# Optimization experiments

Measured on AMD Instinct MI355X. Metric: run time of the kernel, lower is better.

The kernel has to match this reference:

```python
import jax, jax.numpy as jnp
import numpy as np
from jax import lax

DIM = 2048
NUM_HEADS = 16
HEAD_DIM = DIM // NUM_HEADS  # 128
BLOCK = 128
EPS = 1e-6


def setup_inputs() -> dict:
    key = jax.random.key(0)
    kq, kk, kv = jax.random.split(key, 3)
    B, S = 2, 4096
    q = jax.random.normal(kq, (B, S, DIM), dtype=jnp.float32)
    k = jax.random.normal(kk, (B, S, DIM), dtype=jnp.float32)
    v = jax.random.normal(kv, (B, S, DIM), dtype=jnp.float32)
    return {"q": q, "k": k, "v": v}


def _flash_attn(q, k, v):
    # q,k,v: [B, S, DIM] -> [B, H, S, Dh]
    B, S, _ = q.shape
    def split_heads(x):
        return jnp.transpose(x.reshape(B, -1, NUM_HEADS, HEAD_DIM), (0, 2, 1, 3))
    scale = HEAD_DIM ** (-0.5)
    qh = split_heads(q) * scale  # pre-scale, as in original __call__
    kh = split_heads(k)
    vh = split_heads(v)
    Sk = kh.shape[2]
    num_chunks = (Sk + BLOCK - 1) // BLOCK

    o0 = jnp.zeros((B, NUM_HEADS, S, HEAD_DIM), dtype=jnp.float32)
    l0 = jnp.zeros((B, NUM_HEADS, S, 1), dtype=jnp.float32)
    m0 = jnp.full((B, NUM_HEADS, S, 1), -jnp.inf, dtype=jnp.float32)

    def chunk_scanner(carry, chunk_idx):
        o, l, m_run = carry
        start = chunk_idx * BLOCK
        k_c = lax.dynamic_slice(kh, (0, 0, start, 0), (B, NUM_HEADS, BLOCK, HEAD_DIM))
        v_c = lax.dynamic_slice(vh, (0, 0, start, 0), (B, NUM_HEADS, BLOCK, HEAD_DIM))
        # scores: [B, H, Sq, BLOCK]; note second division by sqrt(head_dim) (faithful)
        s = jnp.einsum('bhqd,bhkd->bhqk', qh, k_c,
                       precision=lax.Precision.HIGHEST) / jnp.sqrt(jnp.float32(HEAD_DIM))
        m_chunk = jnp.max(s, axis=-1, keepdims=True)
        m_new = jnp.maximum(m_run, m_chunk)
        exp_scale = jnp.exp(m_run - m_new)
        exp_s = jnp.exp(s - m_chunk)  # faithful: uses m_chunk, not m_new
        l_new = l * exp_scale + jnp.sum(exp_s, axis=-1, keepdims=True)
        o_chunk = jnp.einsum('bhqk,bhkd->bhqd', exp_s, v_c,
                             precision=lax.Precision.HIGHEST)
        o_new = o * exp_scale + o_chunk
        return (o_new, l_new, m_new), None

    (o, l, _), _ = lax.scan(chunk_scanner, (o0, l0, m0), jnp.arange(num_chunks))
    o = o / (l + EPS)
    out = jnp.transpose(o, (0, 2, 1, 3)).reshape(B, -1, DIM)
    return out


def reference(q, k, v):
    return _flash_attn(q, k, v)
```

## Files before the change

### kernel.cpp

```cpp
#include <hip/hip_runtime.h>
#include <hip/hip_bf16.h>
#include <stdint.h>

#define SEQ     4096
#define DMODEL  2048
#define NHEADS  16
#define DHEAD   128
#define QBLK    128
#define CHUNK   128
#define NCHUNK  (SEQ / CHUNK)

typedef __bf16 bf16_t;
typedef bf16_t bf16x8 __attribute__((ext_vector_type(8)));
typedef bf16_t bf16x4 __attribute__((ext_vector_type(4)));
typedef float  f32x4  __attribute__((ext_vector_type(4)));

typedef __attribute__((address_space(3))) uint32_t       lds_u32_t;
typedef __attribute__((address_space(1))) const uint32_t glb_u32_t;

static __device__ __forceinline__ void gload16(const void* g, void* l) {
  __builtin_amdgcn_global_load_lds((glb_u32_t*)g, (lds_u32_t*)l, 16, 0, 0);
}

static __device__ __forceinline__ float exp2_fast(float x) {
  float r;
  asm("v_exp_f32 %0, %1\n\ts_nop 0" : "=v"(r) : "v"(x));
  return r;
}

__device__ __forceinline__ uint32_t swz(int row, int colbyte) {
  return ((uint32_t)(row * 256 + colbyte)) ^ ((uint32_t)(row & 15) << 4);
}

__global__ __launch_bounds__(256)
void prep_k(const float* __restrict__ kk, bf16_t* __restrict__ kb) {
  const size_t e = ((size_t)blockIdx.x * 256 + threadIdx.x) * 8;
  const int dm = (int)(e % DMODEL);
  const int s  = (int)((e / DMODEL) % SEQ);
  const int b  = (int)(e / ((size_t)DMODEL * SEQ));
  float4 x0 = *(const float4*)(kk + e);
  float4 x1 = *(const float4*)(kk + e + 4);
  bf16x8 y;
  y[0]=(bf16_t)x0.x; y[1]=(bf16_t)x0.y; y[2]=(bf16_t)x0.z; y[3]=(bf16_t)x0.w;
  y[4]=(bf16_t)x1.x; y[5]=(bf16_t)x1.y; y[6]=(bf16_t)x1.z; y[7]=(bf16_t)x1.w;
  const size_t out = (((size_t)(b * NHEADS + (dm >> 7)) * SEQ + s) << 7) + (dm & 127);
  *(bf16x8*)(kb + out) = y;
}

__global__ __launch_bounds__(256)
void prep_v(const float* __restrict__ vv, bf16_t* __restrict__ vb) {
  __shared__ bf16_t T[128 * 132];
  const int t = threadIdx.x;
  const int s0 = blockIdx.x * 128, h = blockIdx.y, b = blockIdx.z;
  const float* src = vv + ((size_t)(b * SEQ + s0)) * DMODEL + h * DHEAD;
#pragma unroll
  for (int p = 0; p < 16; ++p) {
    const int sr = p * 8 + (t >> 5), c4 = (t & 31) * 4;
    float4 x = *(const float4*)(src + (size_t)sr * DMODEL + c4);
    bf16_t* d = T + sr * 132 + c4;
    d[0]=(bf16_t)x.x; d[1]=(bf16_t)x.y; d[2]=(bf16_t)x.z; d[3]=(bf16_t)x.w;
  }
  __syncthreads();
  bf16_t* out = vb + ((size_t)(b * NHEADS + h)) * DHEAD * SEQ;
#pragma unroll
  for (int p = 0; p < 8; ++p) {
    const int d = p * 16 + (t >> 4), sc8 = (t & 15) * 8;
    bf16x8 y;
#pragma unroll
    for (int j = 0; j < 8; ++j) y[j] = T[(sc8 + j) * 132 + d];
    *(bf16x8*)(out + (size_t)d * SEQ + s0 + sc8) = y;
  }
}

__global__ __launch_bounds__(512, 2)
void fa_fwd_p(const float* __restrict__ qg, const bf16_t* __restrict__ kbg,
              const bf16_t* __restrict__ vbg, float* __restrict__ og)
{
  __shared__ char smem[65536];

  const int tid  = threadIdx.x;
  const int wave = tid >> 6;
  const int lane = tid & 63;
  const int l15  = lane & 15;
  const int lhi  = lane >> 4;

  const int nwg = gridDim.x * gridDim.y * gridDim.z;
  const int lin = blockIdx.x + gridDim.x * (blockIdx.y + gridDim.y * blockIdx.z);
  const int wg  = (lin % 8) * (nwg / 8) + lin / 8;
  const int bx  = wg % gridDim.x;
  const int h   = (wg / gridDim.x) % NHEADS;
  const int b   = wg / (gridDim.x * NHEADS);
  const int bh  = b * NHEADS + h;
  const int qrow0 = bx * QBLK + wave * 16;

  const bf16_t* kcb = kbg + ((size_t)bh * SEQ) * DHEAD;
  const bf16_t* vcb = vbg + ((size_t)bh * DHEAD) * SEQ;

#define ISSUE_K(koff, key0)                                                    \
  {                                                                            \
    _Pragma("unroll")                                                          \
    for (int u = 0; u < 2; ++u) {                                              \
      const int row = u * 32 + wave * 4 + (lane >> 4);                         \
      const int gl  = lane & 15;                                               \
      const int gx  = (row & 3) | (((row >> 3) & 1) << 2);                     \
      gload16(kcb + (size_t)((key0) + row) * 128 + (gl ^ gx) * 8,              \
              smem + (koff) + u * 8192 + wave * 1024);                         \
    }                                                                          \
  }
#define ISSUE_V(voff, key0)                                                    \
  {                                                                            \
    _Pragma("unroll")                                                          \
    for (int u = 0; u < 2; ++u) {                                              \
      const int dh = u * 64 + wave * 8 + (lane >> 3);                          \
      const int gl = lane & 7;                                                 \
      gload16(vcb + (size_t)dh * SEQ + (key0) + (gl ^ (dh & 7)) * 8,           \
              smem + (voff) + u * 8192 + wave * 1024);                         \
    }                                                                          \
  }

  ISSUE_K(0, 0);
  ISSUE_K(16384, 64);
  ISSUE_V(32768, 0);
  ISSUE_V(49152, 64);

  bf16x8 qa[4];
  {
    const float* qp = qg + ((size_t)(b * SEQ + qrow0 + l15)) * DMODEL + h * DHEAD;
    const float sc = 1.4426950408889634f / 128.0f;
#pragma unroll
    for (int kb = 0; kb < 4; ++kb) {
      const float* p8 = qp + kb * 32 + lhi * 8;
      float4 x0 = *(const float4*)p8;
      float4 x1 = *(const float4*)(p8 + 4);
      bf16x8 a;
      a[0] = (bf16_t)(x0.x * sc); a[1] = (bf16_t)(x0.y * sc);
      a[2] = (bf16_t)(x0.z * sc); a[3] = (bf16_t)(x0.w * sc);
      a[4] = (bf16_t)(x1.x * sc); a[5] = (bf16_t)(x1.y * sc);
      a[6] = (bf16_t)(x1.z * sc); a[7] = (bf16_t)(x1.w * sc);
      qa[kb] = a;
    }
  }

  f32x4 oacc[8];
#pragma unroll
  for (int nt = 0; nt < 8; ++nt) { f32x4 z = {0.f,0.f,0.f,0.f}; oacc[nt] = z; }
  float m_run = -INFINITY;
  float l_run = 0.f;

  asm volatile("s_waitcnt vmcnt(4)\n\ts_barrier" ::: "memory");

  for (int c = 0; c < NCHUNK; ++c) {
    f32x4 sacc[8];
    __builtin_amdgcn_s_setprio(1);
#pragma unroll
    for (int t = 0; t < 2; ++t) {
      const char* Kt = smem + t * 16384;
#pragma unroll
      for (int nl = 0; nl < 4; ++nl) {
        const int rowA = (nl >> 1) * 32 + (l15 >> 2) * 8 + (nl & 1) * 4 + (l15 & 3);
        const int gx   = (rowA & 3) | (((rowA >> 3) & 1) << 2);
        f32x4 acc = {0.f, 0.f, 0.f, 0.f};
#pragma unroll
        for (int j = 0; j < 4; ++j) {
          const uint32_t byte = (uint32_t)(rowA * 256) + ((j * 64 + lhi * 16) ^ (gx << 4));
          bf16x8 kf = *(const bf16x8*)(Kt + byte);
          acc = __builtin_amdgcn_mfma_f32_16x16x32_bf16(kf, qa[j], acc, 0, 0, 0);
        }
        sacc[t * 4 + nl] = acc;
      }
    }
    __builtin_amdgcn_s_setprio(0);

    asm volatile("s_waitcnt vmcnt(0) lgkmcnt(0)\n\ts_barrier" ::: "memory");
    if (c + 1 < NCHUNK) {
      ISSUE_K(0, (c + 1) * CHUNK);
      ISSUE_K(16384, (c + 1) * CHUNK + 64);
    }

    float mc;
    {
      float m0 = sacc[0][0];
#pragma unroll
      for (int i = 0; i < 8; ++i)
#pragma unroll
        for (int r = 0; r < 4; ++r)
          if (i + r) m0 = fmaxf(m0, sacc[i][r]);
      mc = m0;
    }
    mc = fmaxf(mc, __shfl_xor(mc, 16, 64));
    mc = fmaxf(mc, __shfl_xor(mc, 32, 64));

    const float mn = fmaxf(m_run, mc);
    const float e  = exp2_fast(m_run - mn);
    m_run = mn;

    bf16x8 pa[4];
    float ps = 0.f;
#pragma unroll
    for (int nt = 0; nt < 8; ++nt)
#pragma unroll
      for (int r = 0; r < 4; ++r) {
        const float p = exp2_fast(sacc[nt][r] - mc);
        ps += p;
        pa[(nt >> 2) * 2 + ((nt >> 1) & 1)][(nt & 1) * 4 + r] = (bf16_t)p;
      }
    ps += __shfl_xor(ps, 16, 64);
    ps += __shfl_xor(ps, 32, 64);
    l_run = l_run * e + ps;

#pragma unroll
    for (int r = 0; r < 4; ++r) {
      const float er = __shfl(e, lhi * 4 + r, 16);
#pragma unroll
      for (int nt = 0; nt < 8; ++nt) oacc[nt][r] *= er;
    }

    __builtin_amdgcn_s_setprio(1);
#pragma unroll
    for (int kv = 0; kv < 4; ++kv) {
      const char* Vt = smem + 32768 + (kv >> 1) * 16384;
#pragma unroll
      for (int nt = 0; nt < 8; ++nt) {
        const int dh = nt * 16 + l15;
        const uint32_t byte = (uint32_t)(dh * 128) +
            (((kv & 1) * 64 + lhi * 16) ^ ((dh & 7) << 4));
        bf16x8 vf = *(const bf16x8*)(Vt + byte);
        oacc[nt] = __builtin_amdgcn_mfma_f32_16x16x32_bf16(pa[kv], vf, oacc[nt], 0, 0, 0);
      }
    }
    __builtin_amdgcn_s_setprio(0);

    asm volatile("s_waitcnt vmcnt(0) lgkmcnt(0)\n\ts_barrier" ::: "memory");
    if (c + 1 < NCHUNK) {
      ISSUE_V(32768, (c + 1) * CHUNK);
      ISSUE_V(49152, (c + 1) * CHUNK + 64);
    }
  }

  {
    const float lr0 = __shfl(l_run, lhi * 4 + 0, 16);
    const float lr1 = __shfl(l_run, lhi * 4 + 1, 16);
    const float lr2 = __shfl(l_run, lhi * 4 + 2, 16);
    const float lr3 = __shfl(l_run, lhi * 4 + 3, 16);
    const float lr[4] = {lr0, lr1, lr2, lr3};
    char* Ow = smem + wave * 8192;
#pragma unroll
    for (int nt = 0; nt < 8; ++nt)
#pragma unroll
      for (int r = 0; r < 4; ++r) {
        const int row = lhi * 4 + r;
        const int colb = (nt * 16 + l15) * 4;
        *(float*)(Ow + row * 512 + (colb ^ ((row & 7) << 4))) =
            oacc[nt][r] / (lr[r] + 1e-6f);
      }
    asm volatile("s_waitcnt lgkmcnt(0)" ::: "memory");
    __builtin_amdgcn_sched_barrier(0);
#pragma unroll
    for (int p = 0; p < 8; ++p) {
      const int row = p * 2 + (lane >> 5);
      const int colb = (lane & 31) * 16;
      f32x4 val = *(const f32x4*)(Ow + row * 512 + (colb ^ ((row & 7) << 4)));
      *(f32x4*)((char*)(og + ((size_t)(b * SEQ + qrow0 + row)) * DMODEL + h * DHEAD) + colb) = val;
    }
  }
#undef ISSUE_K
#undef ISSUE_V
}

__global__ __launch_bounds__(512, 2)
void fa_fwd_raw(const float* __restrict__ qg, const float* __restrict__ kg,
                const float* __restrict__ vg, float* __restrict__ og)
{
  __shared__ bf16_t Kl[CHUNK * DHEAD];
  __shared__ bf16_t Vt[DHEAD * CHUNK];
  const int tid = threadIdx.x, wave = tid >> 6, lane = tid & 63;
  const int l15 = lane & 15, lhi = lane >> 4;
  const int b = blockIdx.z, h = blockIdx.y;
  const int qrow0 = blockIdx.x * QBLK + wave * 16;
  bf16x8 qa[4];
  {
    const float* qp = qg + ((size_t)(b * SEQ + qrow0 + l15)) * DMODEL + h * DHEAD;
    const float sc = 1.0f / 128.0f;
#pragma unroll
    for (int kb = 0; kb < 4; ++kb) {
      const float* p8 = qp + kb * 32 + lhi * 8;
      float4 x0 = *(const float4*)p8; float4 x1 = *(const float4*)(p8 + 4);
      bf16x8 a;
      a[0]=(bf16_t)(x0.x*sc); a[1]=(bf16_t)(x0.y*sc); a[2]=(bf16_t)(x0.z*sc); a[3]=(bf16_t)(x0.w*sc);
      a[4]=(bf16_t)(x1.x*sc); a[5]=(bf16_t)(x1.y*sc); a[6]=(bf16_t)(x1.z*sc); a[7]=(bf16_t)(x1.w*sc);
      qa[kb] = a;
    }
  }
  f32x4 oacc[8];
#pragma unroll
  for (int nt = 0; nt < 8; ++nt) { f32x4 z = {0.f,0.f,0.f,0.f}; oacc[nt] = z; }
  float m_run[4] = {-INFINITY,-INFINITY,-INFINITY,-INFINITY};
  float l_run[4] = {0.f,0.f,0.f,0.f};
  const float* kbp = kg + ((size_t)b * SEQ) * DMODEL + h * DHEAD;
  const float* vbp = vg + ((size_t)b * SEQ) * DMODEL + h * DHEAD;
  const int krow16 = tid >> 5, kc4 = (tid & 31) * 4;
  const int vdh = tid & 127, vkg = (tid >> 7) * 8;
  for (int c = 0; c < NCHUNK; ++c) {
    const int key0 = c * CHUNK;
#pragma unroll
    for (int pass = 0; pass < 8; ++pass) {
      const int key = pass * 16 + krow16;
      const float4 x = *(const float4*)(kbp + (size_t)(key0 + key) * DMODEL + kc4);
      bf16x4 y; y[0]=(bf16_t)x.x; y[1]=(bf16_t)x.y; y[2]=(bf16_t)x.z; y[3]=(bf16_t)x.w;
      *(bf16x4*)((char*)Kl + swz(key, kc4 * 2)) = y;
    }
#pragma unroll
    for (int it = 0; it < 4; ++it) {
      const int kb0 = it * 32 + vkg;
      const float* vp = vbp + (size_t)(key0 + kb0) * DMODEL + vdh;
      bf16x8 y;
#pragma unroll
      for (int j = 0; j < 8; ++j) y[j] = (bf16_t)vp[(size_t)j * DMODEL];
      *(bf16x8*)((char*)Vt + swz(vdh, kb0 * 2)) = y;
    }
    __syncthreads();
    f32x4 sacc[8];
#pragma unroll
    for (int nt = 0; nt < 8; ++nt) {
      f32x4 acc = {0.f,0.f,0.f,0.f};
      const int key = nt * 16 + l15;
#pragma unroll
      for (int kb = 0; kb < 4; ++kb) {
        bf16x8 bfr = *(const bf16x8*)((const char*)Kl + swz(key, (kb*32+lhi*8)*2));
        acc = __builtin_amdgcn_mfma_f32_16x16x32_bf16(qa[kb], bfr, acc, 0, 0, 0);
      }
      sacc[nt] = acc;
    }
    __syncthreads();
    float mc[4];
#pragma unroll
    for (int r = 0; r < 4; ++r) {
      float m0 = sacc[0][r];
#pragma unroll
      for (int nt = 1; nt < 8; ++nt) m0 = fmaxf(m0, sacc[nt][r]);
      mc[r] = m0;
    }
#pragma unroll
    for (int sh = 1; sh < 16; sh <<= 1)
#pragma unroll
      for (int r = 0; r < 4; ++r) mc[r] = fmaxf(mc[r], __shfl_xor(mc[r], sh, 64));
    float esc[4], psum[4];
#pragma unroll
    for (int r = 0; r < 4; ++r) {
      const float mn = fmaxf(m_run[r], mc[r]);
      esc[r] = __expf(m_run[r] - mn); m_run[r] = mn; psum[r] = 0.f;
    }
    bf16_t* Pw = Kl + wave * (16 * 128);
#pragma unroll
    for (int nt = 0; nt < 8; ++nt)
#pragma unroll
      for (int r = 0; r < 4; ++r) {
        const float p = __expf(sacc[nt][r] - mc[r]);
        psum[r] += p;
        const int row = lhi * 4 + r;
        *(bf16_t*)((char*)Pw + swz(row, (nt*16+l15)*2)) = (bf16_t)p;
      }
#pragma unroll
    for (int sh = 1; sh < 16; sh <<= 1)
#pragma unroll
      for (int r = 0; r < 4; ++r) psum[r] += __shfl_xor(psum[r], sh, 64);
#pragma unroll
    for (int r = 0; r < 4; ++r) l_run[r] = l_run[r] * esc[r] + psum[r];
#pragma unroll
    for (int nt = 0; nt < 8; ++nt) {
      f32x4 o = oacc[nt];
      o[0]*=esc[0]; o[1]*=esc[1]; o[2]*=esc[2]; o[3]*=esc[3];
      oacc[nt] = o;
    }
    asm volatile("s_waitcnt lgkmcnt(0)" ::: "memory");
    __builtin_amdgcn_sched_barrier(0);
#pragma unroll
    for (int kb = 0; kb < 4; ++kb) {
      bf16x8 pf = *(const bf16x8*)((const char*)Pw + swz(l15, (kb*32+lhi*8)*2));
#pragma unroll
      for (int nt = 0; nt < 8; ++nt) {
        const int dh = nt * 16 + l15;
        bf16x8 vf = *(const bf16x8*)((const char*)Vt + swz(dh, (kb*32+lhi*8)*2));
        oacc[nt] = __builtin_amdgcn_mfma_f32_16x16x32_bf16(pf, vf, oacc[nt], 0, 0, 0);
      }
    }
    __syncthreads();
  }
#pragma unroll
  for (int nt = 0; nt < 8; ++nt)
#pragma unroll
    for (int r = 0; r < 4; ++r) {
      const int row = lhi * 4 + r;
      og[((size_t)(b * SEQ + qrow0 + row)) * DMODEL + h * DHEAD + nt * 16 + l15] =
          oacc[nt][r] / (l_run[r] + 1e-6f);
    }
}

extern "C" void kernel_launch(void* const* d_in, const int* in_sizes, int n_in,
                              void* d_out, int out_size, void* d_ws, size_t ws_size,
                              hipStream_t stream) {
  const float* q = (const float*)d_in[0];
  const float* k = (const float*)d_in[1];
  const float* v = (const float*)d_in[2];
  float* o = (float*)d_out;
  const int B = in_sizes[0] / (SEQ * DMODEL);
  const size_t kv_bytes = (size_t)B * NHEADS * SEQ * DHEAD * 2;
  dim3 grid(SEQ / QBLK, NHEADS, B);
  if (ws_size >= 2 * kv_bytes) {
    bf16_t* kb = (bf16_t*)d_ws;
    bf16_t* vb = (bf16_t*)((char*)d_ws + kv_bytes);
    const int nthr = (int)(((size_t)B * SEQ * DMODEL) / 8);
    prep_k<<<nthr / 256, 256, 0, stream>>>(k, kb);
    dim3 gv(SEQ / 128, NHEADS, B);
    prep_v<<<gv, 256, 0, stream>>>(v, vb);
    fa_fwd_p<<<grid, 512, 0, stream>>>(q, kb, vb, o);
  } else {
    fa_fwd_raw<<<grid, 512, 0, stream>>>(q, k, v, o);
  }
}
```

Measured before the change: 339.5 us.

## Process 32 query rows per wave to double K/V reuse per LDS load

Each wave now handles two 16-row query tiles (256 rows per workgroup), so every K and V fragment read from LDS feeds two MFMAs. The V tile is restructured into a single 128-key layout with a 16-way XOR swizzle, and the K swizzle is widened to match. Softmax rescaling of the output accumulator is skipped when the running max does not change. This doubles accumulator registers, drops occupancy to one workgroup per CU, and halves the grid size, which may leave CUs underfilled.

```diff
diff --git a/kernel.cpp b/kernel.cpp
--- a/kernel.cpp
+++ b/kernel.cpp
@@ -6,7 +6,7 @@
 #define DMODEL  2048
 #define NHEADS  16
 #define DHEAD   128
-#define QBLK    128
+#define QBLK    256
 #define CHUNK   128
 #define NCHUNK  (SEQ / CHUNK)
 
@@ -72,7 +72,7 @@
   }
 }
 
-__global__ __launch_bounds__(512, 2)
+__global__ __launch_bounds__(512, 1)
 void fa_fwd_p(const float* __restrict__ qg, const bf16_t* __restrict__ kbg,
               const bf16_t* __restrict__ vbg, float* __restrict__ og)
 {
@@ -91,7 +91,7 @@
   const int h   = (wg / gridDim.x) % NHEADS;
   const int b   = wg / (gridDim.x * NHEADS);
   const int bh  = b * NHEADS + h;
-  const int qrow0 = bx * QBLK + wave * 16;
+  const int qrow0 = bx * QBLK + wave * 32;
 
   const bf16_t* kcb = kbg + ((size_t)bh * SEQ) * DHEAD;
   const bf16_t* vcb = vbg + ((size_t)bh * DHEAD) * SEQ;
@@ -101,56 +101,57 @@
     _Pragma("unroll")                                                          \
     for (int u = 0; u < 2; ++u) {                                              \
       const int row = u * 32 + wave * 4 + (lane >> 4);                         \
-      const int gl  = lane & 15;                                               \
-      const int gx  = (row & 3) | (((row >> 3) & 1) << 2);                     \
-      gload16(kcb + (size_t)((key0) + row) * 128 + (gl ^ gx) * 8,              \
+      const int gx  = (row & 3) | (((row >> 3) & 3) << 2);                     \
+      gload16(kcb + (size_t)((key0) + row) * 128 + (((lane & 15) ^ gx) * 8),   \
               smem + (koff) + u * 8192 + wave * 1024);                         \
     }                                                                          \
   }
-#define ISSUE_V(voff, key0)                                                    \
+#define ISSUE_V(key0)                                                          \
   {                                                                            \
     _Pragma("unroll")                                                          \
-    for (int u = 0; u < 2; ++u) {                                              \
-      const int dh = u * 64 + wave * 8 + (lane >> 3);                          \
-      const int gl = lane & 7;                                                 \
-      gload16(vcb + (size_t)dh * SEQ + (key0) + (gl ^ (dh & 7)) * 8,           \
-              smem + (voff) + u * 8192 + wave * 1024);                         \
+    for (int u = 0; u < 4; ++u) {                                              \
+      const int dh = u * 32 + wave * 4 + (lane >> 4);                          \
+      gload16(vcb + (size_t)dh * SEQ + (key0) + (((lane & 15) ^ (dh & 15)) * 8),\
+              smem + 32768 + u * 8192 + wave * 1024);                          \
     }                                                                          \
   }
 
   ISSUE_K(0, 0);
   ISSUE_K(16384, 64);
-  ISSUE_V(32768, 0);
-  ISSUE_V(49152, 64);
-
-  bf16x8 qa[4];
+  ISSUE_V(0);
+
+  bf16x8 qa[8];
   {
-    const float* qp = qg + ((size_t)(b * SEQ + qrow0 + l15)) * DMODEL + h * DHEAD;
     const float sc = 1.4426950408889634f / 128.0f;
 #pragma unroll
-    for (int kb = 0; kb < 4; ++kb) {
-      const float* p8 = qp + kb * 32 + lhi * 8;
-      float4 x0 = *(const float4*)p8;
-      float4 x1 = *(const float4*)(p8 + 4);
-      bf16x8 a;
-      a[0] = (bf16_t)(x0.x * sc); a[1] = (bf16_t)(x0.y * sc);
-      a[2] = (bf16_t)(x0.z * sc); a[3] = (bf16_t)(x0.w * sc);
-      a[4] = (bf16_t)(x1.x * sc); a[5] = (bf16_t)(x1.y * sc);
-      a[6] = (bf16_t)(x1.z * sc); a[7] = (bf16_t)(x1.w * sc);
-      qa[kb] = a;
-    }
-  }
-
-  f32x4 oacc[8];
-#pragma unroll
-  for (int nt = 0; nt < 8; ++nt) { f32x4 z = {0.f,0.f,0.f,0.f}; oacc[nt] = z; }
-  float m_run = -INFINITY;
-  float l_run = 0.f;
+    for (int h2 = 0; h2 < 2; ++h2) {
+      const float* qp =
+          qg + ((size_t)(b * SEQ + qrow0 + h2 * 16 + l15)) * DMODEL + h * DHEAD;
+#pragma unroll
+      for (int kb = 0; kb < 4; ++kb) {
+        const float* p8 = qp + kb * 32 + lhi * 8;
+        float4 x0 = *(const float4*)p8;
+        float4 x1 = *(const float4*)(p8 + 4);
+        bf16x8 a;
+        a[0] = (bf16_t)(x0.x * sc); a[1] = (bf16_t)(x0.y * sc);
+        a[2] = (bf16_t)(x0.z * sc); a[3] = (bf16_t)(x0.w * sc);
+        a[4] = (bf16_t)(x1.x * sc); a[5] = (bf16_t)(x1.y * sc);
+        a[6] = (bf16_t)(x1.z * sc); a[7] = (bf16_t)(x1.w * sc);
+        qa[h2 * 4 + kb] = a;
+      }
+    }
+  }
+
+  f32x4 oacc[16];
+#pragma unroll
+  for (int nt = 0; nt < 16; ++nt) { f32x4 z = {0.f,0.f,0.f,0.f}; oacc[nt] = z; }
+  float m_run0 = -INFINITY, l_run0 = 0.f;
+  float m_run1 = -INFINITY, l_run1 = 0.f;
 
   asm volatile("s_waitcnt vmcnt(4)\n\ts_barrier" ::: "memory");
 
   for (int c = 0; c < NCHUNK; ++c) {
-    f32x4 sacc[8];
+    f32x4 s0[8], s1[8];
     __builtin_amdgcn_s_setprio(1);
 #pragma unroll
     for (int t = 0; t < 2; ++t) {
@@ -158,15 +159,18 @@
 #pragma unroll
       for (int nl = 0; nl < 4; ++nl) {
         const int rowA = (nl >> 1) * 32 + (l15 >> 2) * 8 + (nl & 1) * 4 + (l15 & 3);
-        const int gx   = (rowA & 3) | (((rowA >> 3) & 1) << 2);
-        f32x4 acc = {0.f, 0.f, 0.f, 0.f};
+        const int gx   = (rowA & 3) | (((rowA >> 3) & 3) << 2);
+        f32x4 a0 = {0.f, 0.f, 0.f, 0.f};
+        f32x4 a1 = {0.f, 0.f, 0.f, 0.f};
 #pragma unroll
         for (int j = 0; j < 4; ++j) {
           const uint32_t byte = (uint32_t)(rowA * 256) + ((j * 64 + lhi * 16) ^ (gx << 4));
           bf16x8 kf = *(const bf16x8*)(Kt + byte);
-          acc = __builtin_amdgcn_mfma_f32_16x16x32_bf16(kf, qa[j], acc, 0, 0, 0);
+          a0 = __builtin_amdgcn_mfma_f32_16x16x32_bf16(kf, qa[j], a0, 0, 0, 0);
+          a1 = __builtin_amdgcn_mfma_f32_16x16x32_bf16(kf, qa[4 + j], a1, 0, 0, 0);
         }
-        sacc[t * 4 + nl] = acc;
+        s0[t * 4 + nl] = a0;
+        s1[t * 4 + nl] = a1;
       }
     }
     __builtin_amdgcn_s_setprio(0);
@@ -177,90 +181,96 @@
       ISSUE_K(16384, (c + 1) * CHUNK + 64);
     }
 
-    float mc;
-    {
-      float m0 = sacc[0][0];
-#pragma unroll
-      for (int i = 0; i < 8; ++i)
-#pragma unroll
-        for (int r = 0; r < 4; ++r)
-          if (i + r) m0 = fmaxf(m0, sacc[i][r]);
-      mc = m0;
-    }
-    mc = fmaxf(mc, __shfl_xor(mc, 16, 64));
-    mc = fmaxf(mc, __shfl_xor(mc, 32, 64));
-
-    const float mn = fmaxf(m_run, mc);
-    const float e  = exp2_fast(m_run - mn);
-    m_run = mn;
-
-    bf16x8 pa[4];
-    float ps = 0.f;
-#pragma unroll
-    for (int nt = 0; nt < 8; ++nt)
-#pragma unroll
-      for (int r = 0; r < 4; ++r) {
-        const float p = exp2_fast(sacc[nt][r] - mc);
-        ps += p;
-        pa[(nt >> 2) * 2 + ((nt >> 1) & 1)][(nt & 1) * 4 + r] = (bf16_t)p;
-      }
-    ps += __shfl_xor(ps, 16, 64);
-    ps += __shfl_xor(ps, 32, 64);
-    l_run = l_run * e + ps;
-
-#pragma unroll
-    for (int r = 0; r < 4; ++r) {
-      const float er = __shfl(e, lhi * 4 + r, 16);
-#pragma unroll
-      for (int nt = 0; nt < 8; ++nt) oacc[nt][r] *= er;
-    }
+    bf16x8 pa0[4], pa1[4];
+#define SOFTMAX_HALF(SA, PA, MRUN, LRUN, OBASE)                                \
+    {                                                                          \
+      float mc = SA[0][0];                                                     \
+      _Pragma("unroll")                                                        \
+      for (int i = 0; i < 8; ++i)                                              \
+        _Pragma("unroll")                                                      \
+        for (int r = 0; r < 4; ++r)                                            \
+          if (i + r) mc = fmaxf(mc, SA[i][r]);                                 \
+      mc = fmaxf(mc, __shfl_xor(mc, 16, 64));                                  \
+      mc = fmaxf(mc, __shfl_xor(mc, 32, 64));                                  \
+      const bool skip = __all(mc <= MRUN);                                     \
+      const float mn = fmaxf(MRUN, mc);                                        \
+      const float e  = exp2_fast(MRUN - mn);                                   \
+      MRUN = mn;                                                               \
+      float ps = 0.f;                                                          \
+      _Pragma("unroll")                                                        \
+      for (int nt = 0; nt < 8; ++nt)                                           \
+        _Pragma("unroll")                                                      \
+        for (int r = 0; r < 4; ++r) {                                          \
+          const float p = exp2_fast(SA[nt][r] - mc);                           \
+          ps += p;                                                             \
+          PA[(nt >> 2) * 2 + ((nt >> 1) & 1)][(nt & 1) * 4 + r] = (bf16_t)p;   \
+        }                                                                      \
+      ps += __shfl_xor(ps, 16, 64);                                            \
+      ps += __shfl_xor(ps, 32, 64);                                            \
+      if (skip) {                                                              \
+        LRUN += ps;                                                            \
+      } else {                                                                 \
+        LRUN = LRUN * e + ps;                                                  \
+        _Pragma("unroll")                                                      \
+        for (int r = 0; r < 4; ++r) {                                          \
+          const float er = __shfl(e, lhi * 4 + r, 16);                         \
+          _Pragma("unroll")                                                    \
+          for (int nt = 0; nt < 8; ++nt) oacc[(OBASE) + nt][r] *= er;          \
+        }                                                                      \
+      }                                                                        \
+    }
+    SOFTMAX_HALF(s0, pa0, m_run0, l_run0, 0)
+    SOFTMAX_HALF(s1, pa1, m_run1, l_run1, 8)
+#undef SOFTMAX_HALF
 
     __builtin_amdgcn_s_setprio(1);
 #pragma unroll
     for (int kv = 0; kv < 4; ++kv) {
-      const char* Vt = smem + 32768 + (kv >> 1) * 16384;
 #pragma unroll
       for (int nt = 0; nt < 8; ++nt) {
         const int dh = nt * 16 + l15;
-        const uint32_t byte = (uint32_t)(dh * 128) +
-            (((kv & 1) * 64 + lhi * 16) ^ ((dh & 7) << 4));
-        bf16x8 vf = *(const bf16x8*)(Vt + byte);
-        oacc[nt] = __builtin_amdgcn_mfma_f32_16x16x32_bf16(pa[kv], vf, oacc[nt], 0, 0, 0);
+        const uint32_t byte = (uint32_t)(32768 + dh * 256) +
+            (((uint32_t)(kv * 64 + lhi * 16)) ^ ((dh & 15) << 4));
+        bf16x8 vf = *(const bf16x8*)(smem + byte);
+        oacc[nt]     = __builtin_amdgcn_mfma_f32_16x16x32_bf16(pa0[kv], vf, oacc[nt], 0, 0, 0);
+        oacc[8 + nt] = __builtin_amdgcn_mfma_f32_16x16x32_bf16(pa1[kv], vf, oacc[8 + nt], 0, 0, 0);
       }
     }
     __builtin_amdgcn_s_setprio(0);
 
     asm volatile("s_waitcnt vmcnt(0) lgkmcnt(0)\n\ts_barrier" ::: "memory");
-    if (c + 1 < NCHUNK) {
-      ISSUE_V(32768, (c + 1) * CHUNK);
-      ISSUE_V(49152, (c + 1) * CHUNK + 64);
-    }
+    if (c + 1 < NCHUNK) ISSUE_V((c + 1) * CHUNK);
   }
 
   {
-    const float lr0 = __shfl(l_run, lhi * 4 + 0, 16);
-    const float lr1 = __shfl(l_run, lhi * 4 + 1, 16);
-    const float lr2 = __shfl(l_run, lhi * 4 + 2, 16);
-    const float lr3 = __shfl(l_run, lhi * 4 + 3, 16);
-    const float lr[4] = {lr0, lr1, lr2, lr3};
     char* Ow = smem + wave * 8192;
 #pragma unroll
-    for (int nt = 0; nt < 8; ++nt)
-#pragma unroll
-      for (int r = 0; r < 4; ++r) {
-        const int row = lhi * 4 + r;
-        const int colb = (nt * 16 + l15) * 4;
-        *(float*)(Ow + row * 512 + (colb ^ ((row & 7) << 4))) =
-            oacc[nt][r] / (lr[r] + 1e-6f);
-      }
-    asm volatile("s_waitcnt lgkmcnt(0)" ::: "memory");
-    __builtin_amdgcn_sched_barrier(0);
-#pragma unroll
-    for (int p = 0; p < 8; ++p) {
-      const int row = p * 2 + (lane >> 5);
-      const int colb = (lane & 31) * 16;
-      f32x4 val = *(const f32x4*)(Ow + row * 512 + (colb ^ ((row & 7) << 4)));
-      *(f32x4*)((char*)(og + ((size_t)(b * SEQ + qrow0 + row)) * DMODEL + h * DHEAD) + colb) = val;
+    for (int h2 = 0; h2 < 2; ++h2) {
+      const float lrl = h2 ? l_run1 : l_run0;
+      float lr[4];
+#pragma unroll
+      for (int r = 0; r < 4; ++r) lr[r] = __shfl(lrl, lhi * 4 + r, 16);
+#pragma unroll
+      for (int nt = 0; nt < 8; ++nt)
+#pragma unroll
+        for (int r = 0; r < 4; ++r) {
+          const int row = lhi * 4 + r;
+          const int colb = (nt * 16 + l15) * 4;
+          *(float*)(Ow + row * 512 + (colb ^ ((row & 7) << 4))) =
+              oacc[h2 * 8 + nt][r] / (lr[r] + 1e-6f);
+        }
+      asm volatile("s_waitcnt lgkmcnt(0)" ::: "memory");
+      __builtin_amdgcn_sched_barrier(0);
+#pragma unroll
+      for (int p = 0; p < 8; ++p) {
+        const int row = p * 2 + (lane >> 5);
+        const int colb = (lane & 31) * 16;
+        f32x4 val = *(const f32x4*)(Ow + row * 512 + (colb ^ ((row & 7) << 4)));
+        *(f32x4*)((char*)(og + ((size_t)(b * SEQ + qrow0 + h2 * 16 + row)) * DMODEL +
+                          h * DHEAD) + colb) = val;
+      }
+      asm volatile("s_waitcnt lgkmcnt(0)" ::: "memory");
+      __builtin_amdgcn_sched_barrier(0);
     }
   }
 #undef ISSUE_K
@@ -276,7 +286,7 @@
   const int tid = threadIdx.x, wave = tid >> 6, lane = tid & 63;
   const int l15 = lane & 15, lhi = lane >> 4;
   const int b = blockIdx.z, h = blockIdx.y;
-  const int qrow0 = blockIdx.x * QBLK + wave * 16;
+  const int qrow0 = blockIdx.x * 128 + wave * 16;
   bf16x8 qa[4];
   {
     const float* qp = qg + ((size_t)(b * SEQ + qrow0 + l15)) * DMODEL + h * DHEAD;
@@ -405,7 +415,6 @@
   float* o = (float*)d_out;
   const int B = in_sizes[0] / (SEQ * DMODEL);
   const size_t kv_bytes = (size_t)B * NHEADS * SEQ * DHEAD * 2;
-  dim3 grid(SEQ / QBLK, NHEADS, B);
   if (ws_size >= 2 * kv_bytes) {
     bf16_t* kb = (bf16_t*)d_ws;
     bf16_t* vb = (bf16_t*)((char*)d_ws + kv_bytes);
@@ -413,8 +422,10 @@
     prep_k<<<nthr / 256, 256, 0, stream>>>(k, kb);
     dim3 gv(SEQ / 128, NHEADS, B);
     prep_v<<<gv, 256, 0, stream>>>(v, vb);
+    dim3 grid(SEQ / QBLK, NHEADS, B);
     fa_fwd_p<<<grid, 512, 0, stream>>>(q, kb, vb, o);
   } else {
+    dim3 grid(SEQ / 128, NHEADS, B);
     fa_fwd_raw<<<grid, 512, 0, stream>>>(q, k, v, o);
   }
 }
```

Result: no change. 335.7 us (-1.1%).

## Read V fragments directly from global memory and skip redundant output rescaling

Applied to the files above, without the earlier changes.

Stops staging V tiles in LDS. Each wave now reads its V MFMA fragments straight from global memory, which halves shared memory to 32 KB and removes the V prefetch and its barrier work. It also widens the K swizzle, uses tree reductions for the row max and sum, skips the O rescale when no row max grew, and writes the output directly instead of bouncing it through LDS. Direct global V loads are uncoalesced strided 16-byte reads exposed on the critical path, so latency and L2 traffic rise in exchange for lower LDS usage.

```diff
diff --git a/kernel.cpp b/kernel.cpp
--- a/kernel.cpp
+++ b/kernel.cpp
@@ -25,6 +25,13 @@
 static __device__ __forceinline__ float exp2_fast(float x) {
   float r;
   asm("v_exp_f32 %0, %1\n\ts_nop 0" : "=v"(r) : "v"(x));
+  return r;
+}
+
+static __device__ __forceinline__ f32x4 vmax4(f32x4 a, f32x4 b) {
+  f32x4 r;
+  r[0] = fmaxf(a[0], b[0]); r[1] = fmaxf(a[1], b[1]);
+  r[2] = fmaxf(a[2], b[2]); r[3] = fmaxf(a[3], b[3]);
   return r;
 }
 
@@ -76,7 +83,7 @@
 void fa_fwd_p(const float* __restrict__ qg, const bf16_t* __restrict__ kbg,
               const bf16_t* __restrict__ vbg, float* __restrict__ og)
 {
-  __shared__ char smem[65536];
+  __shared__ char smem[32768];
 
   const int tid  = threadIdx.x;
   const int wave = tid >> 6;
@@ -101,27 +108,11 @@
     _Pragma("unroll")                                                          \
     for (int u = 0; u < 2; ++u) {                                              \
       const int row = u * 32 + wave * 4 + (lane >> 4);                         \
-      const int gl  = lane & 15;                                               \
-      const int gx  = (row & 3) | (((row >> 3) & 1) << 2);                     \
-      gload16(kcb + (size_t)((key0) + row) * 128 + (gl ^ gx) * 8,              \
+      const int gx  = (row & 3) | (((row >> 3) & 3) << 2);                     \
+      gload16(kcb + (size_t)((key0) + row) * 128 + (((lane & 15) ^ gx) * 8),   \
               smem + (koff) + u * 8192 + wave * 1024);                         \
     }                                                                          \
   }
-#define ISSUE_V(voff, key0)                                                    \
-  {                                                                            \
-    _Pragma("unroll")                                                          \
-    for (int u = 0; u < 2; ++u) {                                              \
-      const int dh = u * 64 + wave * 8 + (lane >> 3);                          \
-      const int gl = lane & 7;                                                 \
-      gload16(vcb + (size_t)dh * SEQ + (key0) + (gl ^ (dh & 7)) * 8,           \
-              smem + (voff) + u * 8192 + wave * 1024);                         \
-    }                                                                          \
-  }
-
-  ISSUE_K(0, 0);
-  ISSUE_K(16384, 64);
-  ISSUE_V(32768, 0);
-  ISSUE_V(49152, 64);
 
   bf16x8 qa[4];
   {
@@ -141,15 +132,20 @@
     }
   }
 
+  ISSUE_K(0, 0);
+  ISSUE_K(16384, 64);
+
   f32x4 oacc[8];
 #pragma unroll
   for (int nt = 0; nt < 8; ++nt) { f32x4 z = {0.f,0.f,0.f,0.f}; oacc[nt] = z; }
   float m_run = -INFINITY;
   float l_run = 0.f;
 
-  asm volatile("s_waitcnt vmcnt(4)\n\ts_barrier" ::: "memory");
+  asm volatile("s_waitcnt vmcnt(0)\n\ts_barrier" ::: "memory");
 
   for (int c = 0; c < NCHUNK; ++c) {
+    const int key0 = c * CHUNK;
+
     f32x4 sacc[8];
     __builtin_amdgcn_s_setprio(1);
 #pragma unroll
@@ -158,7 +154,7 @@
 #pragma unroll
       for (int nl = 0; nl < 4; ++nl) {
         const int rowA = (nl >> 1) * 32 + (l15 >> 2) * 8 + (nl & 1) * 4 + (l15 & 3);
-        const int gx   = (rowA & 3) | (((rowA >> 3) & 1) << 2);
+        const int gx   = (rowA & 3) | (((rowA >> 3) & 3) << 2);
         f32x4 acc = {0.f, 0.f, 0.f, 0.f};
 #pragma unroll
         for (int j = 0; j < 4; ++j) {
@@ -171,100 +167,81 @@
     }
     __builtin_amdgcn_s_setprio(0);
 
-    asm volatile("s_waitcnt vmcnt(0) lgkmcnt(0)\n\ts_barrier" ::: "memory");
+    asm volatile("s_waitcnt lgkmcnt(0)\n\ts_barrier" ::: "memory");
     if (c + 1 < NCHUNK) {
       ISSUE_K(0, (c + 1) * CHUNK);
       ISSUE_K(16384, (c + 1) * CHUNK + 64);
     }
 
-    float mc;
+    bf16x8 pa[4];
     {
-      float m0 = sacc[0][0];
-#pragma unroll
-      for (int i = 0; i < 8; ++i)
-#pragma unroll
-        for (int r = 0; r < 4; ++r)
-          if (i + r) m0 = fmaxf(m0, sacc[i][r]);
-      mc = m0;
-    }
-    mc = fmaxf(mc, __shfl_xor(mc, 16, 64));
-    mc = fmaxf(mc, __shfl_xor(mc, 32, 64));
-
-    const float mn = fmaxf(m_run, mc);
-    const float e  = exp2_fast(m_run - mn);
-    m_run = mn;
-
-    bf16x8 pa[4];
-    float ps = 0.f;
-#pragma unroll
-    for (int nt = 0; nt < 8; ++nt)
-#pragma unroll
-      for (int r = 0; r < 4; ++r) {
-        const float p = exp2_fast(sacc[nt][r] - mc);
-        ps += p;
-        pa[(nt >> 2) * 2 + ((nt >> 1) & 1)][(nt & 1) * 4 + r] = (bf16_t)p;
-      }
-    ps += __shfl_xor(ps, 16, 64);
-    ps += __shfl_xor(ps, 32, 64);
-    l_run = l_run * e + ps;
-
-#pragma unroll
-    for (int r = 0; r < 4; ++r) {
-      const float er = __shfl(e, lhi * 4 + r, 16);
-#pragma unroll
-      for (int nt = 0; nt < 8; ++nt) oacc[nt][r] *= er;
+      f32x4 t0 = vmax4(sacc[0], sacc[1]), t1 = vmax4(sacc[2], sacc[3]);
+      f32x4 t2 = vmax4(sacc[4], sacc[5]), t3 = vmax4(sacc[6], sacc[7]);
+      f32x4 t4 = vmax4(vmax4(t0, t1), vmax4(t2, t3));
+      float mc = fmaxf(fmaxf(fmaxf(t4[0], t4[1]), t4[2]), t4[3]);
+      mc = fmaxf(mc, __shfl_xor(mc, 16, 64));
+      mc = fmaxf(mc, __shfl_xor(mc, 32, 64));
+      const bool skip = __all(mc <= m_run);
+      const float mn = fmaxf(m_run, mc);
+      const float e  = exp2_fast(m_run - mn);
+      m_run = mn;
+      f32x4 pe[8];
+#pragma unroll
+      for (int nt = 0; nt < 8; ++nt)
+#pragma unroll
+        for (int r = 0; r < 4; ++r) {
+          const float p = exp2_fast(sacc[nt][r] - mc);
+          pe[nt][r] = p;
+          pa[(nt >> 2) * 2 + ((nt >> 1) & 1)][(nt & 1) * 4 + r] = (bf16_t)p;
+        }
+      f32x4 q0 = pe[0] + pe[1], q1 = pe[2] + pe[3];
+      f32x4 q2 = pe[4] + pe[5], q3 = pe[6] + pe[7];
+      f32x4 q4 = (q0 + q1) + (q2 + q3);
+      float ps = (q4[0] + q4[1]) + (q4[2] + q4[3]);
+      ps += __shfl_xor(ps, 16, 64);
+      ps += __shfl_xor(ps, 32, 64);
+      if (skip) {
+        l_run += ps;
+      } else {
+        l_run = l_run * e + ps;
+#pragma unroll
+        for (int r = 0; r < 4; ++r) {
+          const float er = __shfl(e, lhi * 4 + r, 16);
+#pragma unroll
+          for (int nt = 0; nt < 8; ++nt) oacc[nt][r] *= er;
+        }
+      }
     }
 
     __builtin_amdgcn_s_setprio(1);
 #pragma unroll
     for (int kv = 0; kv < 4; ++kv) {
-      const char* Vt = smem + 32768 + (kv >> 1) * 16384;
 #pragma unroll
       for (int nt = 0; nt < 8; ++nt) {
-        const int dh = nt * 16 + l15;
-        const uint32_t byte = (uint32_t)(dh * 128) +
-            (((kv & 1) * 64 + lhi * 16) ^ ((dh & 7) << 4));
-        bf16x8 vf = *(const bf16x8*)(Vt + byte);
+        const bf16_t* vp = vcb + (size_t)(nt * 16 + l15) * SEQ + key0 + kv * 32 + lhi * 8;
+        bf16x8 vf = *(const bf16x8*)vp;
         oacc[nt] = __builtin_amdgcn_mfma_f32_16x16x32_bf16(pa[kv], vf, oacc[nt], 0, 0, 0);
       }
     }
     __builtin_amdgcn_s_setprio(0);
 
-    asm volatile("s_waitcnt vmcnt(0) lgkmcnt(0)\n\ts_barrier" ::: "memory");
-    if (c + 1 < NCHUNK) {
-      ISSUE_V(32768, (c + 1) * CHUNK);
-      ISSUE_V(49152, (c + 1) * CHUNK + 64);
-    }
+    asm volatile("s_waitcnt vmcnt(0)\n\ts_barrier" ::: "memory");
   }
 
   {
-    const float lr0 = __shfl(l_run, lhi * 4 + 0, 16);
-    const float lr1 = __shfl(l_run, lhi * 4 + 1, 16);
-    const float lr2 = __shfl(l_run, lhi * 4 + 2, 16);
-    const float lr3 = __shfl(l_run, lhi * 4 + 3, 16);
-    const float lr[4] = {lr0, lr1, lr2, lr3};
-    char* Ow = smem + wave * 8192;
+    float lr[4];
+#pragma unroll
+    for (int r = 0; r < 4; ++r) lr[r] = __shfl(l_run, lhi * 4 + r, 16);
 #pragma unroll
     for (int nt = 0; nt < 8; ++nt)
 #pragma unroll
       for (int r = 0; r < 4; ++r) {
         const int row = lhi * 4 + r;
-        const int colb = (nt * 16 + l15) * 4;
-        *(float*)(Ow + row * 512 + (colb ^ ((row & 7) << 4))) =
+        og[((size_t)(b * SEQ + qrow0 + row)) * DMODEL + h * DHEAD + nt * 16 + l15] =
             oacc[nt][r] / (lr[r] + 1e-6f);
       }
-    asm volatile("s_waitcnt lgkmcnt(0)" ::: "memory");
-    __builtin_amdgcn_sched_barrier(0);
-#pragma unroll
-    for (int p = 0; p < 8; ++p) {
-      const int row = p * 2 + (lane >> 5);
-      const int colb = (lane & 31) * 16;
-      f32x4 val = *(const f32x4*)(Ow + row * 512 + (colb ^ ((row & 7) << 4)));
-      *(f32x4*)((char*)(og + ((size_t)(b * SEQ + qrow0 + row)) * DMODEL + h * DHEAD) + colb) = val;
-    }
   }
 #undef ISSUE_K
-#undef ISSUE_V
 }
 
 __global__ __launch_bounds__(512, 2)
@@ -276,7 +253,7 @@
   const int tid = threadIdx.x, wave = tid >> 6, lane = tid & 63;
   const int l15 = lane & 15, lhi = lane >> 4;
   const int b = blockIdx.z, h = blockIdx.y;
-  const int qrow0 = blockIdx.x * QBLK + wave * 16;
+  const int qrow0 = blockIdx.x * 128 + wave * 16;
   bf16x8 qa[4];
   {
     const float* qp = qg + ((size_t)(b * SEQ + qrow0 + l15)) * DMODEL + h * DHEAD;
@@ -405,7 +382,6 @@
   float* o = (float*)d_out;
   const int B = in_sizes[0] / (SEQ * DMODEL);
   const size_t kv_bytes = (size_t)B * NHEADS * SEQ * DHEAD * 2;
-  dim3 grid(SEQ / QBLK, NHEADS, B);
   if (ws_size >= 2 * kv_bytes) {
     bf16_t* kb = (bf16_t*)d_ws;
     bf16_t* vb = (bf16_t*)((char*)d_ws + kv_bytes);
@@ -413,8 +389,10 @@
     prep_k<<<nthr / 256, 256, 0, stream>>>(k, kb);
     dim3 gv(SEQ / 128, NHEADS, B);
     prep_v<<<gv, 256, 0, stream>>>(v, vb);
+    dim3 grid(SEQ / QBLK, NHEADS, B);
     fa_fwd_p<<<grid, 512, 0, stream>>>(q, kb, vb, o);
   } else {
+    dim3 grid(SEQ / 128, NHEADS, B);
     fa_fwd_raw<<<grid, 512, 0, stream>>>(q, k, v, o);
   }
 }
```

New measurement: 1.035 ms. +204.8%, slower.
